# Kernel tuning notes

Hardware: AMD Instinct MI355X
Metric: run time of the kernel (lower is better)

The kernel has to match this reference:

```python
import jax, jax.numpy as jnp
import numpy as np

B, R, C, NNZ = 128, 8192, 16384, 524288


def setup_inputs() -> dict:
    key = jax.random.key(0)
    k1, k2, k3, k4 = jax.random.split(key, 4)
    x_batched = jax.random.normal(k1, (B, C), dtype=jnp.float32)
    M_vals = jax.random.normal(k2, (NNZ,), dtype=jnp.float32)
    M_row_idx = jax.random.randint(k3, (NNZ,), 0, R, dtype=jnp.int32)
    M_col_idx = jax.random.randint(k4, (NNZ,), 0, C, dtype=jnp.int32)
    return {
        "x_batched": x_batched,
        "M_vals": M_vals,
        "M_row_idx": M_row_idx,
        "M_col_idx": M_col_idx,
    }


def reference(x_batched, M_vals, M_row_idx, M_col_idx):
    # Batched SpMM in COO form: y[b, r] = sum_k vals[k] * x[b, cols[k]] where rows[k]==r.
    # Replaces the original per-sample tf.map_fn loop with one vectorized gather + segment_sum.
    gathered = x_batched[:, M_col_idx] * M_vals  # [B, NNZ]
    y = jax.ops.segment_sum(gathered.T, M_row_idx, num_segments=R)  # [R, B]
    return y.T  # [B, R]
```

## Files before the change

kernel.cpp:

```cpp
#include <hip/hip_runtime.h>
#include <hip/hip_bf16.h>

#define BN 128
#define RN 8192
#define CN 16384
#define CAP 192

__device__ __forceinline__ unsigned bf16hi(float f) {
    unsigned u = __float_as_uint(f);
    unsigned r = u + 0x7FFFu + ((u >> 16) & 1u);
    return r & 0xFFFF0000u;
}

__global__ void __launch_bounds__(256) txpose_cvt_kernel(
        const float* __restrict__ x, unsigned short* __restrict__ xT,
        int* __restrict__ counts) {
    if (blockIdx.x < 2048) {
        __shared__ unsigned short tile[32][34];
        int cBase = (blockIdx.x & 511) * 32;
        int bBase = (blockIdx.x >> 9) * 32;
        int tx = threadIdx.x & 31;
        int ty = threadIdx.x >> 5;
        #pragma unroll
        for (int i = ty; i < 32; i += 8) {
            float f = x[(size_t)(bBase + i) * CN + cBase + tx];
            tile[tx][i] = (unsigned short)(bf16hi(f) >> 16);
        }
        __syncthreads();
        #pragma unroll
        for (int it = 0; it < 2; ++it) {
            int idx = it * 256 + threadIdx.x;
            int bl = (idx & 15) * 2;
            int cl = idx >> 4;
            unsigned v = (unsigned)tile[cl][bl] | ((unsigned)tile[cl][bl + 1] << 16);
            *reinterpret_cast<unsigned*>(&xT[(size_t)(cBase + cl) * BN + bBase + bl]) = v;
        }
    } else {
        int i = (blockIdx.x - 2048) * 256 + threadIdx.x;
        counts[i] = 0;
    }
}

__global__ void __launch_bounds__(256) scatter_kernel(
        const int* __restrict__ rows, const int* __restrict__ cols,
        const float* __restrict__ vals,
        int* __restrict__ counts, unsigned* __restrict__ pk, int nnz) {
    int i = (blockIdx.x * 256 + threadIdx.x) * 2;
    if (i < nnz) {
        int2   rr = *reinterpret_cast<const int2*>(&rows[i]);
        int2   cc = *reinterpret_cast<const int2*>(&cols[i]);
        float2 vv = *reinterpret_cast<const float2*>(&vals[i]);
        int p0 = atomicAdd(&counts[rr.x], 1);
        if (p0 < CAP) pk[(size_t)rr.x * CAP + p0] = bf16hi(vv.x) | (unsigned)cc.x;
        int p1 = atomicAdd(&counts[rr.y], 1);
        if (p1 < CAP) pk[(size_t)rr.y * CAP + p1] = bf16hi(vv.y) | (unsigned)cc.y;
    }
}

#define SPMM_BODY(EJ, A0, A1)                                          \
    {                                                                  \
        unsigned c_ = (EJ) & 0xFFFFu;                                  \
        float    v_ = __uint_as_float((EJ) & 0xFFFF0000u);             \
        unsigned d_ = xw[c_ * (BN / 2) + t];                           \
        A0 += v_ * __uint_as_float(d_ << 16);                          \
        A1 += v_ * __uint_as_float(d_ & 0xFFFF0000u);                  \
    }

__global__ void __launch_bounds__(512) spmm_kernel(
        const unsigned short* __restrict__ xT,
        const int* __restrict__ counts,
        const unsigned* __restrict__ pk,
        float* __restrict__ out) {
    __shared__ float tile[8][136];
    const unsigned* xw = reinterpret_cast<const unsigned*>(xT);
    int t = threadIdx.x & 63;
    int w = threadIdx.x >> 6;
    int r = blockIdx.x * 8 + w;
    int cnt = counts[r]; cnt = cnt < CAP ? cnt : CAP;
    const unsigned* prow = pk + (size_t)r * CAP;

    float a0 = 0.f, a1 = 0.f, a2 = 0.f, a3 = 0.f;

    int base = 0;
    while (base + 64 <= cnt) {
        unsigned e = prow[base + t];
        #pragma unroll 8
        for (int j = 0; j < 64; j += 2) {
            unsigned e0 = (unsigned)__builtin_amdgcn_readlane((int)e, j);
            unsigned e1 = (unsigned)__builtin_amdgcn_readlane((int)e, j + 1);
            SPMM_BODY(e0, a0, a1)
            SPMM_BODY(e1, a2, a3)
        }
        base += 64;
    }
    int rem = cnt - base;
    if (rem > 0) {
        unsigned e = (t < rem) ? prow[base + t] : 0u;
        if (rem <= 32) {
            #pragma unroll 8
            for (int j = 0; j < 32; j += 2) {
                unsigned e0 = (unsigned)__builtin_amdgcn_readlane((int)e, j);
                unsigned e1 = (unsigned)__builtin_amdgcn_readlane((int)e, j + 1);
                SPMM_BODY(e0, a0, a1)
                SPMM_BODY(e1, a2, a3)
            }
        } else {
            #pragma unroll 8
            for (int j = 0; j < 64; j += 2) {
                unsigned e0 = (unsigned)__builtin_amdgcn_readlane((int)e, j);
                unsigned e1 = (unsigned)__builtin_amdgcn_readlane((int)e, j + 1);
                SPMM_BODY(e0, a0, a1)
                SPMM_BODY(e1, a2, a3)
            }
        }
    }

    tile[w][2 * t]     = a0 + a2;
    tile[w][2 * t + 1] = a1 + a3;
    __syncthreads();
    #pragma unroll
    for (int it = 0; it < 2; ++it) {
        int idx = it * 512 + (int)threadIdx.x;
        int r8 = idx & 7;
        int b  = idx >> 3;
        out[(size_t)b * RN + blockIdx.x * 8 + r8] = tile[r8][b];
    }
}

extern "C" void kernel_launch(void* const* d_in, const int* in_sizes, int n_in,
                              void* d_out, int out_size, void* d_ws, size_t ws_size,
                              hipStream_t stream) {
    const float* x    = (const float*)d_in[0];
    const float* vals = (const float*)d_in[1];
    const int*   rows = (const int*)d_in[2];
    const int*   cols = (const int*)d_in[3];
    float*       out  = (float*)d_out;
    const int nnz = in_sizes[1];

    char* ws = (char*)d_ws;
    unsigned short* xT = (unsigned short*)ws;
    unsigned* pk       = (unsigned*)(ws + (size_t)CN * BN * 2);
    int* counts        = (int*)(ws + (size_t)CN * BN * 2 + (size_t)RN * CAP * 4);

    txpose_cvt_kernel<<<2048 + RN / 256, 256, 0, stream>>>(x, xT, counts);

    scatter_kernel<<<(nnz / 2 + 255) / 256, 256, 0, stream>>>(
        rows, cols, vals, counts, pk, nnz);

    spmm_kernel<<<RN / 8, 512, 0, stream>>>(xT, counts, pk, out);
}
```

Before: 50.18 us.

## Fuse transpose and COO scatter into one prep kernel, prefetch entries in SpMM

The bf16 transpose of x and the atomic COO-to-bucket scatter now run in a single launch, with each scatter thread handling four nonzeros through vectorized loads. Count zeroing moves to a hipMemsetAsync. The SpMM loop prefetches the next 64 packed entries while processing the current ones, folds the tail handling into one path, raises the unroll factor, adds an occupancy hint to launch bounds, and writes output with nontemporal stores. This trades one kernel launch for a memset node and puts pressure on register usage through the deeper unroll and prefetch.

```diff
diff --git a/kernel.cpp b/kernel.cpp
--- a/kernel.cpp
+++ b/kernel.cpp
@@ -12,9 +12,11 @@
     return r & 0xFFFF0000u;
 }
 
-__global__ void __launch_bounds__(256) txpose_cvt_kernel(
+__global__ void __launch_bounds__(256) prep_kernel(
         const float* __restrict__ x, unsigned short* __restrict__ xT,
-        int* __restrict__ counts) {
+        const int* __restrict__ rows, const int* __restrict__ cols,
+        const float* __restrict__ vals,
+        int* __restrict__ counts, unsigned* __restrict__ pk, int nnz) {
     if (blockIdx.x < 2048) {
         __shared__ unsigned short tile[32][34];
         int cBase = (blockIdx.x & 511) * 32;
@@ -36,37 +38,49 @@
             *reinterpret_cast<unsigned*>(&xT[(size_t)(cBase + cl) * BN + bBase + bl]) = v;
         }
     } else {
-        int i = (blockIdx.x - 2048) * 256 + threadIdx.x;
-        counts[i] = 0;
+        int i = ((blockIdx.x - 2048) * 256 + threadIdx.x) * 4;
+        if (i < nnz) {
+            int4   rr = *reinterpret_cast<const int4*>(&rows[i]);
+            int4   cc = *reinterpret_cast<const int4*>(&cols[i]);
+            float4 vv = *reinterpret_cast<const float4*>(&vals[i]);
+            int p;
+            p = atomicAdd(&counts[rr.x], 1);
+            if (p < CAP) pk[(size_t)rr.x * CAP + p] = bf16hi(vv.x) | (unsigned)cc.x;
+            p = atomicAdd(&counts[rr.y], 1);
+            if (p < CAP) pk[(size_t)rr.y * CAP + p] = bf16hi(vv.y) | (unsigned)cc.y;
+            p = atomicAdd(&counts[rr.z], 1);
+            if (p < CAP) pk[(size_t)rr.z * CAP + p] = bf16hi(vv.z) | (unsigned)cc.z;
+            p = atomicAdd(&counts[rr.w], 1);
+            if (p < CAP) pk[(size_t)rr.w * CAP + p] = bf16hi(vv.w) | (unsigned)cc.w;
+        }
     }
 }
 
-__global__ void __launch_bounds__(256) scatter_kernel(
-        const int* __restrict__ rows, const int* __restrict__ cols,
-        const float* __restrict__ vals,
-        int* __restrict__ counts, unsigned* __restrict__ pk, int nnz) {
-    int i = (blockIdx.x * 256 + threadIdx.x) * 2;
-    if (i < nnz) {
-        int2   rr = *reinterpret_cast<const int2*>(&rows[i]);
-        int2   cc = *reinterpret_cast<const int2*>(&cols[i]);
-        float2 vv = *reinterpret_cast<const float2*>(&vals[i]);
-        int p0 = atomicAdd(&counts[rr.x], 1);
-        if (p0 < CAP) pk[(size_t)rr.x * CAP + p0] = bf16hi(vv.x) | (unsigned)cc.x;
-        int p1 = atomicAdd(&counts[rr.y], 1);
-        if (p1 < CAP) pk[(size_t)rr.y * CAP + p1] = bf16hi(vv.y) | (unsigned)cc.y;
-    }
-}
-
-#define SPMM_BODY(EJ, A0, A1)                                          \
-    {                                                                  \
-        unsigned c_ = (EJ) & 0xFFFFu;                                  \
-        float    v_ = __uint_as_float((EJ) & 0xFFFF0000u);             \
-        unsigned d_ = xw[c_ * (BN / 2) + t];                           \
-        A0 += v_ * __uint_as_float(d_ << 16);                          \
-        A1 += v_ * __uint_as_float(d_ & 0xFFFF0000u);                  \
+#define BODY2(EU0, EU1)                                                 \
+    {                                                                   \
+        unsigned c0_ = (EU0) & 0xFFFFu;                                 \
+        float    v0_ = __uint_as_float((EU0) & 0xFFFF0000u);            \
+        unsigned c1_ = (EU1) & 0xFFFFu;                                 \
+        float    v1_ = __uint_as_float((EU1) & 0xFFFF0000u);            \
+        unsigned d0_ = xw[c0_ * (BN / 2) + t];                          \
+        unsigned d1_ = xw[c1_ * (BN / 2) + t];                          \
+        a0 += v0_ * __uint_as_float(d0_ << 16);                         \
+        a1 += v0_ * __uint_as_float(d0_ & 0xFFFF0000u);                 \
+        a2 += v1_ * __uint_as_float(d1_ << 16);                         \
+        a3 += v1_ * __uint_as_float(d1_ & 0xFFFF0000u);                 \
     }
 
-__global__ void __launch_bounds__(512) spmm_kernel(
+#define PROC(N_)                                                        \
+    {                                                                   \
+        _Pragma("unroll 16")                                            \
+        for (int j = 0; j < (N_); j += 2) {                             \
+            unsigned e0 = (unsigned)__builtin_amdgcn_readlane((int)e, j);     \
+            unsigned e1 = (unsigned)__builtin_amdgcn_readlane((int)e, j + 1); \
+            BODY2(e0, e1)                                               \
+        }                                                               \
+    }
+
+__global__ void __launch_bounds__(512, 8) spmm_kernel(
         const unsigned short* __restrict__ xT,
         const int* __restrict__ counts,
         const unsigned* __restrict__ pk,
@@ -81,39 +95,16 @@
 
     float a0 = 0.f, a1 = 0.f, a2 = 0.f, a3 = 0.f;
 
+    unsigned e = (t < cnt) ? prow[t] : 0u;
     int base = 0;
-    while (base + 64 <= cnt) {
-        unsigned e = prow[base + t];
-        #pragma unroll 8
-        for (int j = 0; j < 64; j += 2) {
-            unsigned e0 = (unsigned)__builtin_amdgcn_readlane((int)e, j);
-            unsigned e1 = (unsigned)__builtin_amdgcn_readlane((int)e, j + 1);
-            SPMM_BODY(e0, a0, a1)
-            SPMM_BODY(e1, a2, a3)
-        }
+    while (base + 64 < cnt) {
+        int nrem = cnt - base - 64;
+        unsigned enext = (t < nrem) ? prow[base + 64 + t] : 0u;
+        PROC(64)
+        e = enext;
         base += 64;
     }
-    int rem = cnt - base;
-    if (rem > 0) {
-        unsigned e = (t < rem) ? prow[base + t] : 0u;
-        if (rem <= 32) {
-            #pragma unroll 8
-            for (int j = 0; j < 32; j += 2) {
-                unsigned e0 = (unsigned)__builtin_amdgcn_readlane((int)e, j);
-                unsigned e1 = (unsigned)__builtin_amdgcn_readlane((int)e, j + 1);
-                SPMM_BODY(e0, a0, a1)
-                SPMM_BODY(e1, a2, a3)
-            }
-        } else {
-            #pragma unroll 8
-            for (int j = 0; j < 64; j += 2) {
-                unsigned e0 = (unsigned)__builtin_amdgcn_readlane((int)e, j);
-                unsigned e1 = (unsigned)__builtin_amdgcn_readlane((int)e, j + 1);
-                SPMM_BODY(e0, a0, a1)
-                SPMM_BODY(e1, a2, a3)
-            }
-        }
-    }
+    if (cnt - base > 32) { PROC(64) } else { PROC(32) }
 
     tile[w][2 * t]     = a0 + a2;
     tile[w][2 * t + 1] = a1 + a3;
@@ -123,7 +114,8 @@
         int idx = it * 512 + (int)threadIdx.x;
         int r8 = idx & 7;
         int b  = idx >> 3;
-        out[(size_t)b * RN + blockIdx.x * 8 + r8] = tile[r8][b];
+        __builtin_nontemporal_store(tile[r8][b],
+                                    &out[(size_t)b * RN + blockIdx.x * 8 + r8]);
     }
 }
 
@@ -142,10 +134,10 @@
     unsigned* pk       = (unsigned*)(ws + (size_t)CN * BN * 2);
     int* counts        = (int*)(ws + (size_t)CN * BN * 2 + (size_t)RN * CAP * 4);
 
-    txpose_cvt_kernel<<<2048 + RN / 256, 256, 0, stream>>>(x, xT, counts);
+    hipMemsetAsync(counts, 0, RN * sizeof(int), stream);
 
-    scatter_kernel<<<(nnz / 2 + 255) / 256, 256, 0, stream>>>(
-        rows, cols, vals, counts, pk, nnz);
+    prep_kernel<<<2048 + (nnz + 1023) / 1024, 256, 0, stream>>>(
+        x, xT, rows, cols, vals, counts, pk, nnz);
 
     spmm_kernel<<<RN / 8, 512, 0, stream>>>(xT, counts, pk, out);
 }
```

Measured after the change: 56.49 us. +12.6%, slower.

## Fuse transpose and COO scatter into one kernel, zeroing counts separately

Applied to the files above, without the earlier changes.

The x transpose/bf16 conversion and the COO scatter into per-row buckets now run as different block ranges of a single prep kernel, so both phases overlap on the device. A tiny separate kernel zeroes the row counters first. The scatter path also handles four nonzeros per thread with 128-bit loads instead of two. This is meant to cut one launch boundary and fill idle CUs, at the cost of an extra small launch and more atomics per thread.

```diff
diff --git a/kernel.cpp b/kernel.cpp
--- a/kernel.cpp
+++ b/kernel.cpp
@@ -12,9 +12,15 @@
     return r & 0xFFFF0000u;
 }
 
-__global__ void __launch_bounds__(256) txpose_cvt_kernel(
+__global__ void __launch_bounds__(256) zero_kernel(int4* __restrict__ counts4) {
+    counts4[blockIdx.x * 256 + threadIdx.x] = make_int4(0, 0, 0, 0);
+}
+
+__global__ void __launch_bounds__(256) prep_kernel(
         const float* __restrict__ x, unsigned short* __restrict__ xT,
-        int* __restrict__ counts) {
+        const int* __restrict__ rows, const int* __restrict__ cols,
+        const float* __restrict__ vals,
+        int* __restrict__ counts, unsigned* __restrict__ pk, int nnz) {
     if (blockIdx.x < 2048) {
         __shared__ unsigned short tile[32][34];
         int cBase = (blockIdx.x & 511) * 32;
@@ -36,24 +42,21 @@
             *reinterpret_cast<unsigned*>(&xT[(size_t)(cBase + cl) * BN + bBase + bl]) = v;
         }
     } else {
-        int i = (blockIdx.x - 2048) * 256 + threadIdx.x;
-        counts[i] = 0;
-    }
-}
-
-__global__ void __launch_bounds__(256) scatter_kernel(
-        const int* __restrict__ rows, const int* __restrict__ cols,
-        const float* __restrict__ vals,
-        int* __restrict__ counts, unsigned* __restrict__ pk, int nnz) {
-    int i = (blockIdx.x * 256 + threadIdx.x) * 2;
-    if (i < nnz) {
-        int2   rr = *reinterpret_cast<const int2*>(&rows[i]);
-        int2   cc = *reinterpret_cast<const int2*>(&cols[i]);
-        float2 vv = *reinterpret_cast<const float2*>(&vals[i]);
-        int p0 = atomicAdd(&counts[rr.x], 1);
-        if (p0 < CAP) pk[(size_t)rr.x * CAP + p0] = bf16hi(vv.x) | (unsigned)cc.x;
-        int p1 = atomicAdd(&counts[rr.y], 1);
-        if (p1 < CAP) pk[(size_t)rr.y * CAP + p1] = bf16hi(vv.y) | (unsigned)cc.y;
+        int i = ((blockIdx.x - 2048) * 256 + threadIdx.x) * 4;
+        if (i < nnz) {
+            int4   rr = *reinterpret_cast<const int4*>(&rows[i]);
+            int4   cc = *reinterpret_cast<const int4*>(&cols[i]);
+            float4 vv = *reinterpret_cast<const float4*>(&vals[i]);
+            int p;
+            p = atomicAdd(&counts[rr.x], 1);
+            if (p < CAP) pk[(size_t)rr.x * CAP + p] = bf16hi(vv.x) | (unsigned)cc.x;
+            p = atomicAdd(&counts[rr.y], 1);
+            if (p < CAP) pk[(size_t)rr.y * CAP + p] = bf16hi(vv.y) | (unsigned)cc.y;
+            p = atomicAdd(&counts[rr.z], 1);
+            if (p < CAP) pk[(size_t)rr.z * CAP + p] = bf16hi(vv.z) | (unsigned)cc.z;
+            p = atomicAdd(&counts[rr.w], 1);
+            if (p < CAP) pk[(size_t)rr.w * CAP + p] = bf16hi(vv.w) | (unsigned)cc.w;
+        }
     }
 }
 
@@ -142,10 +145,10 @@
     unsigned* pk       = (unsigned*)(ws + (size_t)CN * BN * 2);
     int* counts        = (int*)(ws + (size_t)CN * BN * 2 + (size_t)RN * CAP * 4);
 
-    txpose_cvt_kernel<<<2048 + RN / 256, 256, 0, stream>>>(x, xT, counts);
+    zero_kernel<<<RN / 1024, 256, 0, stream>>>((int4*)counts);
 
-    scatter_kernel<<<(nnz / 2 + 255) / 256, 256, 0, stream>>>(
-        rows, cols, vals, counts, pk, nnz);
+    prep_kernel<<<2048 + (nnz + 1023) / 1024, 256, 0, stream>>>(
+        x, xT, rows, cols, vals, counts, pk, nnz);
 
     spmm_kernel<<<RN / 8, 512, 0, stream>>>(xT, counts, pk, out);
 }
```

New measurement: 54.03 us. 7.7% more time.
